# Kernel tuning notes

Measured on AMD Instinct MI355X. Metric: run time of the kernel, lower is better.

## Reference

```python
import jax, jax.numpy as jnp
import numpy as np

LN_EPS = 1e-5

def setup_inputs() -> dict:
    key = jax.random.key(0)
    B, T, D, H, NB = 32, 384, 512, 16, 5  # NB = 5 MHSA blocks actually used
    ks = jax.random.split(key, 10)
    s = 1.0 / np.sqrt(D)
    def w(k, shape):
        return jax.random.normal(k, shape, jnp.float32) * s
    return {
        "x": jax.random.normal(ks[0], (B, T, D), jnp.float32),
        # stacked params for the 5 used MHSA blocks, order:
        # [tmp_attn, layer1_1, layer1_2, layer1_3, layer2_1]
        "qw": w(ks[1], (NB, D, D)), "qb": w(ks[2], (NB, D)),
        "kw": w(ks[3], (NB, D, D)), "kb": w(ks[4], (NB, D)),
        "vw": w(ks[5], (NB, D, D)), "vb": w(ks[6], (NB, D)),
        "temp": jnp.ones((NB, H, 1, 1), jnp.float32),
        "ln_g": jnp.ones((D,), jnp.float32),
        "ln_b": jnp.zeros((D,), jnp.float32),
        "fus_w": w(ks[7], (D, D)), "fus_b": w(ks[8], (D,)),
        "num_heads": H,
    }


def _mhsa(x, wq, bq, wk, bk, wv, bv, temp, H):
    # Faithful to torch: .view(B, H, D//H, T) is a flat reshape of (B,T,D).
    B, T, D = x.shape
    d = D // H
    q = (x @ wq.T + bq).reshape(B, H, d, T)
    k = (x @ wk.T + bk).reshape(B, H, d, T)
    v = (x @ wv.T + bv).reshape(B, H, d, T)
    # k^T @ v -> (B,H,T,T), scaled by per-head temperature, softmax over last dim
    attn = jax.nn.softmax(jnp.einsum("bhdt,bhds->bhts", k, v) * temp, axis=-1)
    out = jnp.einsum("bhdt,bhts->bhds", q, attn)  # (B,H,d,T)
    return out.reshape(B, T, D)


def _layernorm(x, g, b):
    mu = jnp.mean(x, axis=-1, keepdims=True)
    var = jnp.mean(jnp.square(x - mu), axis=-1, keepdims=True)
    return (x - mu) * jax.lax.rsqrt(var + LN_EPS) * g + b


def reference(x, qw, qb, kw, kb, vw, vb, temp, ln_g, ln_b, fus_w, fus_b, num_heads):
    H = num_heads
    blk = lambda i, z: _mhsa(z, qw[i], qb[i], kw[i], kb[i], vw[i], vb[i], temp[i], H)
    x_ = blk(0, x)
    c1, c2, c3 = jnp.split(x, 3, axis=1)
    tmp_layer1 = jnp.concatenate([blk(1, c1), blk(2, c2), blk(3, c3)], axis=1) + x_
    tmp_layer2 = blk(4, _layernorm(tmp_layer1, ln_g, ln_b)) + x_
    alpha = jnp.stack([tmp_layer1, tmp_layer2], axis=0)  # (2,B,T,D)
    alpha = alpha @ fus_w.T + fus_b
    alpha = jax.nn.softmax(alpha, axis=0)
    return tmp_layer1 * alpha[0] + tmp_layer2 * alpha[1]
```

## Files before the change

### kernel.cpp

```cpp
#include <hip/hip_runtime.h>

typedef __attribute__((ext_vector_type(8))) _Float16 half8;
typedef __attribute__((ext_vector_type(4))) _Float16 half4v;
typedef __attribute__((ext_vector_type(4))) float float4v;

__device__ __forceinline__ float4v mfma16x16x32_f16(half8 a, half8 b, float4v c) {
#if defined(__HIP_DEVICE_COMPILE__)
#if __has_builtin(__builtin_amdgcn_mfma_f32_16x16x32_f16)
  return __builtin_amdgcn_mfma_f32_16x16x32_f16(a, b, c, 0, 0, 0);
#elif __has_builtin(__builtin_amdgcn_mfma_f32_16x16x32f16)
  return __builtin_amdgcn_mfma_f32_16x16x32f16(a, b, c, 0, 0, 0);
#else
#error "no 16x16x32 f16 mfma"
#endif
#else
  (void)a; (void)b;
  return c;
#endif
}

__device__ __forceinline__ float4v mfma16x16x16_f16(half4v a, half4v b, float4v c) {
#if defined(__HIP_DEVICE_COMPILE__)
#if __has_builtin(__builtin_amdgcn_mfma_f32_16x16x16f16)
  return __builtin_amdgcn_mfma_f32_16x16x16f16(a, b, c, 0, 0, 0);
#elif __has_builtin(__builtin_amdgcn_mfma_f32_16x16x16_f16)
  return __builtin_amdgcn_mfma_f32_16x16x16_f16(a, b, c, 0, 0, 0);
#else
#error "no 16x16x16 f16 mfma"
#endif
#else
  (void)a; (void)b;
  return c;
#endif
}

__device__ __forceinline__ void gl_lds16(const unsigned short* g, unsigned short* l) {
#if defined(__HIP_DEVICE_COMPILE__)
#if __has_builtin(__builtin_amdgcn_global_load_lds)
  __builtin_amdgcn_global_load_lds(
      (const __attribute__((address_space(1))) unsigned int*)g,
      (__attribute__((address_space(3))) unsigned int*)l, 16, 0, 0);
#else
  *(uint4*)l = *(const uint4*)g;
#endif
#else
  (void)g; (void)l;
#endif
}

__device__ __forceinline__ float fexp2(float x) {
#if defined(__HIP_DEVICE_COMPILE__)
#if __has_builtin(__builtin_amdgcn_exp2f)
  return __builtin_amdgcn_exp2f(x);
#else
  return __expf(x * 0.6931471805599453f);
#endif
#else
  return x;
#endif
}

__device__ __forceinline__ unsigned short f2h(float f) {
  union { _Float16 h; unsigned short u; } v;
  v.h = (_Float16)f;
  return v.u;
}

__global__ __launch_bounds__(256) void cvt_f32_f16(const float* __restrict__ in,
                                                   unsigned short* __restrict__ out, int n4) {
  int i = blockIdx.x * 256 + threadIdx.x;
  if (i >= n4) return;
  float4 v = ((const float4*)in)[i];
  uint2 o;
  o.x = (unsigned)f2h(v.x) | ((unsigned)f2h(v.y) << 16);
  o.y = (unsigned)f2h(v.z) | ((unsigned)f2h(v.w) << 16);
  ((uint2*)out)[i] = o;
}

#define GEMM_K_LOOP(XPTR, WPTR)                                                        \
  const int sw = col & 7;                                                              \
  for (int k0 = 0; k0 < 512; k0 += 64) {                                               \
    const unsigned short* Xg = (XPTR) + k0;                                            \
    const unsigned short* Wg = (WPTR) + k0;                                            \
    _Pragma("unroll") for (int rnd = 0; rnd < 4; ++rnd) {                              \
      const int slot = rnd * 256 + tid;                                                \
      const int r = slot >> 3;                                                         \
      const int c = (slot & 7) ^ (r & 7);                                              \
      gl_lds16(Xg + (size_t)r * 512 + c * 8, &Xs[slot * 8]);                           \
      gl_lds16(Wg + (size_t)r * 512 + c * 8, &Wt[slot * 8]);                           \
    }                                                                                  \
    __syncthreads();                                                                   \
    _Pragma("unroll") for (int kk = 0; kk < 2; ++kk) {                                 \
      half8 af[4], bf[4];                                                              \
      _Pragma("unroll") for (int i = 0; i < 4; ++i) {                                  \
        const int r = wm + i * 16 + col;                                               \
        af[i] = *(const half8*)&Xs[r * 64 + ((kk * 4 + grp) ^ sw) * 8];                \
      }                                                                                \
      _Pragma("unroll") for (int j = 0; j < 4; ++j) {                                  \
        const int r = wn + j * 16 + col;                                               \
        bf[j] = *(const half8*)&Wt[r * 64 + ((kk * 4 + grp) ^ sw) * 8];                \
      }                                                                                \
      _Pragma("unroll") for (int i = 0; i < 4; ++i)                                    \
          _Pragma("unroll") for (int j = 0; j < 4; ++j)                                \
              acc[i][j] = mfma16x16x32_f16(af[i], bf[j], acc[i][j]);                   \
    }                                                                                  \
    __syncthreads();                                                                   \
  }

__global__ __launch_bounds__(256) void gemm_qkv(
    const unsigned short* __restrict__ X,
    const unsigned short* __restrict__ Wq, const unsigned short* __restrict__ Wk,
    const unsigned short* __restrict__ Wv,
    const float* __restrict__ bq, const float* __restrict__ bk, const float* __restrict__ bv,
    unsigned short* __restrict__ Cq, unsigned short* __restrict__ Ck, unsigned short* __restrict__ Cv,
    int wsel_mode, int widx_fixed) {
  const int nt = blockIdx.x, mt = blockIdx.y, z = blockIdx.z;
  const unsigned short* W = (z == 0) ? Wq : ((z == 1) ? Wk : Wv);
  const float* bias = (z == 0) ? bq : ((z == 1) ? bk : bv);
  unsigned short* C = (z == 0) ? Cq : ((z == 1) ? Ck : Cv);
  const int widx = wsel_mode ? (1 + (mt % 3)) : widx_fixed;
  W += (size_t)widx * 512 * 512;
  bias += widx * 512;

  __shared__ __align__(16) unsigned short Xs[128 * 64];
  __shared__ __align__(16) unsigned short Wt[128 * 64];
  const int tid = threadIdx.x, lane = tid & 63, w = tid >> 6;
  const int col = lane & 15, grp = lane >> 4;
  const int wm = (w >> 1) * 64, wn = (w & 1) * 64;

  const float4v zero4 = {0.f, 0.f, 0.f, 0.f};
  float4v acc[4][4];
#pragma unroll
  for (int i = 0; i < 4; ++i)
#pragma unroll
    for (int j = 0; j < 4; ++j) acc[i][j] = zero4;

  GEMM_K_LOOP(X + (size_t)mt * 128 * 512, W + (size_t)nt * 128 * 512)

#pragma unroll
  for (int j = 0; j < 4; ++j) {
    const int n = nt * 128 + wn + j * 16 + col;
    const float bj = bias[n];
#pragma unroll
    for (int i = 0; i < 4; ++i)
#pragma unroll
      for (int r = 0; r < 4; ++r) {
        const int m = mt * 128 + wm + i * 16 + grp * 4 + r;
        C[(size_t)m * 512 + n] = f2h(acc[i][j][r] + bj);
      }
  }
}

__global__ __launch_bounds__(256) void gemm_fusion(
    const unsigned short* __restrict__ X, const unsigned short* __restrict__ Wf,
    const float* __restrict__ tl1, const float* __restrict__ tl2, float* __restrict__ outp) {
  const int nt = blockIdx.x, mt = blockIdx.y;
  __shared__ __align__(16) unsigned short Xs[128 * 64];
  __shared__ __align__(16) unsigned short Wt[128 * 64];
  const int tid = threadIdx.x, lane = tid & 63, w = tid >> 6;
  const int col = lane & 15, grp = lane >> 4;
  const int wm = (w >> 1) * 64, wn = (w & 1) * 64;

  const float4v zero4 = {0.f, 0.f, 0.f, 0.f};
  float4v acc[4][4];
#pragma unroll
  for (int i = 0; i < 4; ++i)
#pragma unroll
    for (int j = 0; j < 4; ++j) acc[i][j] = zero4;

  GEMM_K_LOOP(X + (size_t)mt * 128 * 512, Wf + (size_t)nt * 128 * 512)

#pragma unroll
  for (int j = 0; j < 4; ++j) {
    const int n = nt * 128 + wn + j * 16 + col;
#pragma unroll
    for (int i = 0; i < 4; ++i)
#pragma unroll
      for (int r = 0; r < 4; ++r) {
        const int m = mt * 128 + wm + i * 16 + grp * 4 + r;
        const size_t off = (size_t)m * 512 + n;
        const float t1 = tl1[off], t2 = tl2[off];
        const float sg = 1.0f / (1.0f + __expf(-acc[i][j][r]));
        outp[off] = t2 + (t1 - t2) * sg;
      }
  }
}

template <int T>
__global__ __launch_bounds__(512) void attn_kernel(
    const unsigned short* __restrict__ Qb, const unsigned short* __restrict__ Kb,
    const unsigned short* __restrict__ Vb, const float* __restrict__ temp_base,
    const float* add_src,
    float* outp, int chunk_elems,
    const float* __restrict__ tl1_src, unsigned short* __restrict__ diff_out) {
  constexpr int NT = T / 16;
  constexpr int NSW = (T / 16) / 8;
  constexpr int SLAB = T * 32;
  const int h = blockIdx.x, b = blockIdx.y, cb = blockIdx.z;
  const int base = b * (384 * 512) + cb * chunk_elems + h * SLAB;
  const float tl2e = temp_base[cb * 16 + h] * 1.4426950408889634f;

  __shared__ __align__(16) unsigned short KVt[T][40];
  __shared__ __align__(16) float Zp[2][2][8][16];

  const int tid = threadIdx.x, lane = tid & 63, w = tid >> 6;
  const int col = lane & 15, grp = lane >> 4;

  auto stage = [&](const unsigned short* src) {
    constexpr int ITER = (T * 4) / 512;
#pragma unroll
    for (int p = 0; p < ITER; ++p) {
      const int f = p * 512 + tid;
      const int t = f >> 2, blk = (f & 3) * 8;
      unsigned short tmp[8];
#pragma unroll
      for (int i = 0; i < 8; ++i) tmp[i] = src[(size_t)(blk + i) * T + t];
      *(uint4*)&KVt[t][blk] = *(const uint4*)tmp;
    }
  };

  stage(Vb + base);
  __syncthreads();
  half8 vfr[NSW];
#pragma unroll
  for (int si = 0; si < NSW; ++si)
    vfr[si] = *(const half8*)&KVt[(w + si * 8) * 16 + col][grp * 8];
  __syncthreads();
  stage(Kb + base);
  __syncthreads();

  const float4v zero4 = {0.f, 0.f, 0.f, 0.f};
  const unsigned short* Qsl = Qb + base;
  float4v oacc[NSW][2];
#pragma unroll
  for (int si = 0; si < NSW; ++si) {
    oacc[si][0] = zero4;
    oacc[si][1] = zero4;
  }

  for (int kk = 0; kk < NT / 2; ++kk) {
    const int par = kk & 1;
    float pe[2][NSW][4];
#pragma unroll
    for (int u = 0; u < 2; ++u) {
      const int tt = kk * 2 + u;
      half8 kf = *(const half8*)&KVt[tt * 16 + col][grp * 8];
      float z0 = 0.f, z1 = 0.f, z2 = 0.f, z3 = 0.f;
#pragma unroll
      for (int si = 0; si < NSW; ++si) {
        float4v s = mfma16x16x32_f16(kf, vfr[si], zero4);
        pe[u][si][0] = fexp2(s[0] * tl2e);
        pe[u][si][1] = fexp2(s[1] * tl2e);
        pe[u][si][2] = fexp2(s[2] * tl2e);
        pe[u][si][3] = fexp2(s[3] * tl2e);
        z0 += pe[u][si][0];
        z1 += pe[u][si][1];
        z2 += pe[u][si][2];
        z3 += pe[u][si][3];
      }
#pragma unroll
      for (int m = 1; m < 16; m <<= 1) {
        z0 += __shfl_xor(z0, m);
        z1 += __shfl_xor(z1, m);
        z2 += __shfl_xor(z2, m);
        z3 += __shfl_xor(z3, m);
      }
      if (col == 0) {
        float4v zv = {z0, z1, z2, z3};
        *(float4v*)&Zp[par][u][w][grp * 4] = zv;
      }
    }
    half4v qa[2][2];
#pragma unroll
    for (int u = 0; u < 2; ++u) {
      const int toff = (kk * 2 + u) * 16 + grp * 4;
      qa[u][0] = *(const half4v*)(Qsl + col * T + toff);
      qa[u][1] = *(const half4v*)(Qsl + (16 + col) * T + toff);
    }
    __syncthreads();
#pragma unroll
    for (int u = 0; u < 2; ++u) {
      float4v zs = zero4;
#pragma unroll
      for (int ww = 0; ww < 8; ++ww) zs += *(const float4v*)&Zp[par][u][ww][grp * 4];
      const float zi0 = 1.0f / zs[0], zi1 = 1.0f / zs[1], zi2 = 1.0f / zs[2],
                  zi3 = 1.0f / zs[3];
#pragma unroll
      for (int si = 0; si < NSW; ++si) {
        half4v pb;
        pb[0] = (_Float16)(pe[u][si][0] * zi0);
        pb[1] = (_Float16)(pe[u][si][1] * zi1);
        pb[2] = (_Float16)(pe[u][si][2] * zi2);
        pb[3] = (_Float16)(pe[u][si][3] * zi3);
        oacc[si][0] = mfma16x16x16_f16(qa[u][0], pb, oacc[si][0]);
        oacc[si][1] = mfma16x16x16_f16(qa[u][1], pb, oacc[si][1]);
      }
    }
  }

#pragma unroll
  for (int si = 0; si < NSW; ++si) {
    const int s = (w + si * 8) * 16 + col;
#pragma unroll
    for (int m0 = 0; m0 < 2; ++m0) {
#pragma unroll
      for (int r = 0; r < 4; ++r) {
        const int dd = m0 * 16 + grp * 4 + r;
        const int off = base + dd * T + s;
        float v = oacc[si][m0][r];
        if (add_src) v += add_src[off];
        outp[off] = v;
        if (diff_out) diff_out[off] = f2h(tl1_src[off] - v);
      }
    }
  }
}

__global__ __launch_bounds__(256) void ln_kernel(const float* __restrict__ xin,
                                                 const float* __restrict__ g,
                                                 const float* __restrict__ bb,
                                                 unsigned short* __restrict__ y) {
  const int row = blockIdx.x * 4 + (threadIdx.x >> 6);
  const int lane = threadIdx.x & 63;
  const float* xr = xin + (size_t)row * 512;
  float4 v0 = *(const float4*)&xr[lane * 8];
  float4 v1 = *(const float4*)&xr[lane * 8 + 4];
  float s = v0.x + v0.y + v0.z + v0.w + v1.x + v1.y + v1.z + v1.w;
  float q = v0.x * v0.x + v0.y * v0.y + v0.z * v0.z + v0.w * v0.w +
            v1.x * v1.x + v1.y * v1.y + v1.z * v1.z + v1.w * v1.w;
#pragma unroll
  for (int m = 1; m < 64; m <<= 1) {
    s += __shfl_xor(s, m);
    q += __shfl_xor(q, m);
  }
  const float mean = s * (1.0f / 512.0f);
  const float var = q * (1.0f / 512.0f) - mean * mean;
  const float rs = rsqrtf(var + 1e-5f);
  float4 g0 = *(const float4*)&g[lane * 8];
  float4 g1 = *(const float4*)&g[lane * 8 + 4];
  float4 b0 = *(const float4*)&bb[lane * 8];
  float4 b1 = *(const float4*)&bb[lane * 8 + 4];
  uint4 o;
  o.x = (unsigned)f2h((v0.x - mean) * rs * g0.x + b0.x) |
        ((unsigned)f2h((v0.y - mean) * rs * g0.y + b0.y) << 16);
  o.y = (unsigned)f2h((v0.z - mean) * rs * g0.z + b0.z) |
        ((unsigned)f2h((v0.w - mean) * rs * g0.w + b0.w) << 16);
  o.z = (unsigned)f2h((v1.x - mean) * rs * g1.x + b1.x) |
        ((unsigned)f2h((v1.y - mean) * rs * g1.y + b1.y) << 16);
  o.w = (unsigned)f2h((v1.z - mean) * rs * g1.z + b1.z) |
        ((unsigned)f2h((v1.w - mean) * rs * g1.w + b1.w) << 16);
  *(uint4*)&y[(size_t)row * 512 + lane * 8] = o;
}

extern "C" void kernel_launch(void* const* d_in, const int* in_sizes, int n_in,
                              void* d_out, int out_size, void* d_ws, size_t ws_size,
                              hipStream_t stream) {
  const float* x = (const float*)d_in[0];
  const float* qw = (const float*)d_in[1];
  const float* qb = (const float*)d_in[2];
  const float* kw = (const float*)d_in[3];
  const float* kb = (const float*)d_in[4];
  const float* vw = (const float*)d_in[5];
  const float* vb = (const float*)d_in[6];
  const float* temp = (const float*)d_in[7];
  const float* ln_g = (const float*)d_in[8];
  const float* ln_b = (const float*)d_in[9];
  const float* fus_w = (const float*)d_in[10];
  float* out = (float*)d_out;

  const size_t NE = (size_t)32 * 384 * 512;
  const size_t WE = (size_t)5 * 512 * 512;

  char* p = (char*)d_ws;
  auto alloc = [&](size_t bytes) {
    char* r = p;
    p += (bytes + 255) & ~(size_t)255;
    return r;
  };
  unsigned short* xb = (unsigned short*)alloc(NE * 2);
  unsigned short* wqb = (unsigned short*)alloc(WE * 2);
  unsigned short* wkb = (unsigned short*)alloc(WE * 2);
  unsigned short* wvb = (unsigned short*)alloc(WE * 2);
  unsigned short* fwb = (unsigned short*)alloc((size_t)512 * 512 * 2);
  unsigned short* Qb = (unsigned short*)alloc(NE * 2);
  unsigned short* Kb = (unsigned short*)alloc(NE * 2);
  unsigned short* Vb = (unsigned short*)alloc(NE * 2);
  float* xres = (float*)alloc(NE * 4);
  float* tl1 = (float*)alloc(NE * 4);
  unsigned short* yb = (unsigned short*)alloc(NE * 2);

  cvt_f32_f16<<<(int)((NE / 4 + 255) / 256), 256, 0, stream>>>(x, xb, (int)(NE / 4));
  cvt_f32_f16<<<(int)((WE / 4 + 255) / 256), 256, 0, stream>>>(qw, wqb, (int)(WE / 4));
  cvt_f32_f16<<<(int)((WE / 4 + 255) / 256), 256, 0, stream>>>(kw, wkb, (int)(WE / 4));
  cvt_f32_f16<<<(int)((WE / 4 + 255) / 256), 256, 0, stream>>>(vw, wvb, (int)(WE / 4));
  cvt_f32_f16<<<256, 256, 0, stream>>>(fus_w, fwb, 512 * 512 / 4);

  gemm_qkv<<<dim3(4, 96, 3), 256, 0, stream>>>(xb, wqb, wkb, wvb, qb, kb, vb, Qb, Kb, Vb, 0, 0);
  attn_kernel<384><<<dim3(16, 32, 1), 512, 0, stream>>>(Qb, Kb, Vb, temp, nullptr, xres, 0,
                                                        nullptr, nullptr);
  gemm_qkv<<<dim3(4, 96, 3), 256, 0, stream>>>(xb, wqb, wkb, wvb, qb, kb, vb, Qb, Kb, Vb, 1, 0);
  attn_kernel<128><<<dim3(16, 32, 3), 512, 0, stream>>>(Qb, Kb, Vb, temp + 16, xres, tl1,
                                                        128 * 512, nullptr, nullptr);
  ln_kernel<<<12288 / 4, 256, 0, stream>>>(tl1, ln_g, ln_b, yb);
  gemm_qkv<<<dim3(4, 96, 3), 256, 0, stream>>>(yb, wqb, wkb, wvb, qb, kb, vb, Qb, Kb, Vb, 0, 4);
  attn_kernel<384><<<dim3(16, 32, 1), 512, 0, stream>>>(Qb, Kb, Vb, temp + 64, xres, xres, 0,
                                                        tl1, yb);
  gemm_fusion<<<dim3(4, 96, 1), 256, 0, stream>>>(yb, fwb, tl1, xres, out);

  (void)in_sizes; (void)n_in; (void)out_size; (void)ws_size;
}
```

Before: 413.6 us.

## Enlarge GEMM tiles to 256 rows with 512 threads, batch attention softmax groups

The GEMM kernels now use 512-thread blocks that each compute 256 rows (two 128-row segments that can be non-contiguous, so the per-chunk weight selection is kept) against a 128-column weight tile. This halves the grid and reuses each loaded weight tile across twice as many rows. The attention kernel processes NB t-tiles per barrier group (4 for T=384) instead of 2, cutting syncthreads count, and packs probabilities to f16 with cvt_pkrtz. The larger tiles and groups raise register and LDS pressure and leave fewer blocks to spread across CUs. Round-toward-zero packing slightly changes rounding.

```diff
diff --git a/kernel.cpp b/kernel.cpp
--- a/kernel.cpp
+++ b/kernel.cpp
@@ -2,6 +2,7 @@
 
 typedef __attribute__((ext_vector_type(8))) _Float16 half8;
 typedef __attribute__((ext_vector_type(4))) _Float16 half4v;
+typedef __attribute__((ext_vector_type(2))) _Float16 half2v;
 typedef __attribute__((ext_vector_type(4))) float float4v;
 
 __device__ __forceinline__ float4v mfma16x16x32_f16(half8 a, half8 b, float4v c) {
@@ -57,6 +58,24 @@
 #endif
 #else
   return x;
+#endif
+}
+
+__device__ __forceinline__ half2v pk_f16(float a, float b) {
+#if defined(__HIP_DEVICE_COMPILE__)
+#if __has_builtin(__builtin_amdgcn_cvt_pkrtz)
+  return __builtin_bit_cast(half2v, __builtin_amdgcn_cvt_pkrtz(a, b));
+#else
+  half2v r;
+  r[0] = (_Float16)a;
+  r[1] = (_Float16)b;
+  return r;
+#endif
+#else
+  half2v r;
+  r[0] = (_Float16)a;
+  r[1] = (_Float16)b;
+  return r;
 #endif
 }
 
@@ -77,29 +96,30 @@
   ((uint2*)out)[i] = o;
 }
 
-#define GEMM_K_LOOP(XPTR, WPTR)                                                        \
-  const int sw = col & 7;                                                              \
+#define GEMM_CORE(WGPTR)                                                               \
   for (int k0 = 0; k0 < 512; k0 += 64) {                                               \
-    const unsigned short* Xg = (XPTR) + k0;                                            \
-    const unsigned short* Wg = (WPTR) + k0;                                            \
     _Pragma("unroll") for (int rnd = 0; rnd < 4; ++rnd) {                              \
-      const int slot = rnd * 256 + tid;                                                \
+      const int slot = rnd * 512 + tid;                                                \
       const int r = slot >> 3;                                                         \
       const int c = (slot & 7) ^ (r & 7);                                              \
-      gl_lds16(Xg + (size_t)r * 512 + c * 8, &Xs[slot * 8]);                           \
-      gl_lds16(Wg + (size_t)r * 512 + c * 8, &Wt[slot * 8]);                           \
+      const size_t src = ((r >> 7) ? xrow1 : xrow0) + (size_t)(r & 127) * 512 +        \
+                         (size_t)(k0 + c * 8);                                         \
+      gl_lds16(Xbase + src, &Xs[slot * 8]);                                            \
+    }                                                                                  \
+    _Pragma("unroll") for (int rnd = 0; rnd < 2; ++rnd) {                              \
+      const int s2 = rnd * 512 + tid;                                                  \
+      const int r = s2 >> 3;                                                           \
+      const int c = (s2 & 7) ^ (r & 7);                                                \
+      gl_lds16((WGPTR) + (size_t)r * 512 + k0 + c * 8, &Wt[s2 * 8]);                   \
     }                                                                                  \
     __syncthreads();                                                                   \
     _Pragma("unroll") for (int kk = 0; kk < 2; ++kk) {                                 \
       half8 af[4], bf[4];                                                              \
-      _Pragma("unroll") for (int i = 0; i < 4; ++i) {                                  \
-        const int r = wm + i * 16 + col;                                               \
-        af[i] = *(const half8*)&Xs[r * 64 + ((kk * 4 + grp) ^ sw) * 8];                \
-      }                                                                                \
-      _Pragma("unroll") for (int j = 0; j < 4; ++j) {                                  \
-        const int r = wn + j * 16 + col;                                               \
-        bf[j] = *(const half8*)&Wt[r * 64 + ((kk * 4 + grp) ^ sw) * 8];                \
-      }                                                                                \
+      const int ch = ((kk * 4 + grp) ^ (col & 7)) * 8;                                 \
+      _Pragma("unroll") for (int i = 0; i < 4; ++i)                                    \
+          af[i] = *(const half8*)&Xs[(wm + i * 16 + col) * 64 + ch];                   \
+      _Pragma("unroll") for (int j = 0; j < 4; ++j)                                    \
+          bf[j] = *(const half8*)&Wt[(wn + j * 16 + col) * 64 + ch];                   \
       _Pragma("unroll") for (int i = 0; i < 4; ++i)                                    \
           _Pragma("unroll") for (int j = 0; j < 4; ++j)                                \
               acc[i][j] = mfma16x16x32_f16(af[i], bf[j], acc[i][j]);                   \
@@ -107,7 +127,7 @@
     __syncthreads();                                                                   \
   }
 
-__global__ __launch_bounds__(256) void gemm_qkv(
+__global__ __launch_bounds__(512) void gemm_qkv(
     const unsigned short* __restrict__ X,
     const unsigned short* __restrict__ Wq, const unsigned short* __restrict__ Wk,
     const unsigned short* __restrict__ Wv,
@@ -118,12 +138,18 @@
   const unsigned short* W = (z == 0) ? Wq : ((z == 1) ? Wk : Wv);
   const float* bias = (z == 0) ? bq : ((z == 1) ? bk : bv);
   unsigned short* C = (z == 0) ? Cq : ((z == 1) ? Ck : Cv);
-  const int widx = wsel_mode ? (1 + (mt % 3)) : widx_fixed;
+  const int cpart = mt % 3, bb = (mt / 3) * 2;
+  const int widx = wsel_mode ? (1 + cpart) : widx_fixed;
   W += (size_t)widx * 512 * 512;
   bias += widx * 512;
 
-  __shared__ __align__(16) unsigned short Xs[128 * 64];
-  __shared__ __align__(16) unsigned short Wt[128 * 64];
+  const size_t grow0 = (size_t)bb * 384 + cpart * 128;
+  const size_t grow1 = grow0 + 384;
+  const size_t xrow0 = grow0 * 512, xrow1 = grow1 * 512;
+  const unsigned short* Xbase = X;
+
+  __shared__ __align__(16) unsigned short Xs[2048 * 8];
+  __shared__ __align__(16) unsigned short Wt[1024 * 8];
   const int tid = threadIdx.x, lane = tid & 63, w = tid >> 6;
   const int col = lane & 15, grp = lane >> 4;
   const int wm = (w >> 1) * 64, wn = (w & 1) * 64;
@@ -135,7 +161,7 @@
 #pragma unroll
     for (int j = 0; j < 4; ++j) acc[i][j] = zero4;
 
-  GEMM_K_LOOP(X + (size_t)mt * 128 * 512, W + (size_t)nt * 128 * 512)
+  GEMM_CORE(W + (size_t)nt * 128 * 512)
 
 #pragma unroll
   for (int j = 0; j < 4; ++j) {
@@ -145,18 +171,23 @@
     for (int i = 0; i < 4; ++i)
 #pragma unroll
       for (int r = 0; r < 4; ++r) {
-        const int m = mt * 128 + wm + i * 16 + grp * 4 + r;
-        C[(size_t)m * 512 + n] = f2h(acc[i][j][r] + bj);
-      }
-  }
-}
-
-__global__ __launch_bounds__(256) void gemm_fusion(
+        const int m = wm + i * 16 + grp * 4 + r;
+        const size_t grow = ((m >> 7) ? grow1 : grow0) + (m & 127);
+        C[grow * 512 + n] = f2h(acc[i][j][r] + bj);
+      }
+  }
+}
+
+__global__ __launch_bounds__(512) void gemm_fusion(
     const unsigned short* __restrict__ X, const unsigned short* __restrict__ Wf,
     const float* __restrict__ tl1, const float* __restrict__ tl2, float* __restrict__ outp) {
   const int nt = blockIdx.x, mt = blockIdx.y;
-  __shared__ __align__(16) unsigned short Xs[128 * 64];
-  __shared__ __align__(16) unsigned short Wt[128 * 64];
+  const size_t grow0 = (size_t)mt * 256, grow1 = grow0 + 128;
+  const size_t xrow0 = grow0 * 512, xrow1 = grow1 * 512;
+  const unsigned short* Xbase = X;
+
+  __shared__ __align__(16) unsigned short Xs[2048 * 8];
+  __shared__ __align__(16) unsigned short Wt[1024 * 8];
   const int tid = threadIdx.x, lane = tid & 63, w = tid >> 6;
   const int col = lane & 15, grp = lane >> 4;
   const int wm = (w >> 1) * 64, wn = (w & 1) * 64;
@@ -168,7 +199,7 @@
 #pragma unroll
     for (int j = 0; j < 4; ++j) acc[i][j] = zero4;
 
-  GEMM_K_LOOP(X + (size_t)mt * 128 * 512, Wf + (size_t)nt * 128 * 512)
+  GEMM_CORE(Wf + (size_t)nt * 128 * 512)
 
 #pragma unroll
   for (int j = 0; j < 4; ++j) {
@@ -177,8 +208,8 @@
     for (int i = 0; i < 4; ++i)
 #pragma unroll
       for (int r = 0; r < 4; ++r) {
-        const int m = mt * 128 + wm + i * 16 + grp * 4 + r;
-        const size_t off = (size_t)m * 512 + n;
+        const int m = wm + i * 16 + grp * 4 + r;
+        const size_t off = (((m >> 7) ? grow1 : grow0) + (m & 127)) * 512 + n;
         const float t1 = tl1[off], t2 = tl2[off];
         const float sg = 1.0f / (1.0f + __expf(-acc[i][j][r]));
         outp[off] = t2 + (t1 - t2) * sg;
@@ -186,7 +217,7 @@
   }
 }
 
-template <int T>
+template <int T, int NB>
 __global__ __launch_bounds__(512) void attn_kernel(
     const unsigned short* __restrict__ Qb, const unsigned short* __restrict__ Kb,
     const unsigned short* __restrict__ Vb, const float* __restrict__ temp_base,
@@ -201,7 +232,7 @@
   const float tl2e = temp_base[cb * 16 + h] * 1.4426950408889634f;
 
   __shared__ __align__(16) unsigned short KVt[T][40];
-  __shared__ __align__(16) float Zp[2][2][8][16];
+  __shared__ __align__(16) float Zp[2][NB][8][16];
 
   const int tid = threadIdx.x, lane = tid & 63, w = tid >> 6;
   const int col = lane & 15, grp = lane >> 4;
@@ -238,12 +269,12 @@
     oacc[si][1] = zero4;
   }
 
-  for (int kk = 0; kk < NT / 2; ++kk) {
-    const int par = kk & 1;
-    float pe[2][NSW][4];
-#pragma unroll
-    for (int u = 0; u < 2; ++u) {
-      const int tt = kk * 2 + u;
+  for (int g = 0; g < NT / NB; ++g) {
+    const int par = g & 1;
+    float pe[NB][NSW][4];
+#pragma unroll
+    for (int u = 0; u < NB; ++u) {
+      const int tt = g * NB + u;
       half8 kf = *(const half8*)&KVt[tt * 16 + col][grp * 8];
       float z0 = 0.f, z1 = 0.f, z2 = 0.f, z3 = 0.f;
 #pragma unroll
@@ -270,16 +301,16 @@
         *(float4v*)&Zp[par][u][w][grp * 4] = zv;
       }
     }
-    half4v qa[2][2];
-#pragma unroll
-    for (int u = 0; u < 2; ++u) {
-      const int toff = (kk * 2 + u) * 16 + grp * 4;
+    half4v qa[NB][2];
+#pragma unroll
+    for (int u = 0; u < NB; ++u) {
+      const int toff = (g * NB + u) * 16 + grp * 4;
       qa[u][0] = *(const half4v*)(Qsl + col * T + toff);
       qa[u][1] = *(const half4v*)(Qsl + (16 + col) * T + toff);
     }
     __syncthreads();
 #pragma unroll
-    for (int u = 0; u < 2; ++u) {
+    for (int u = 0; u < NB; ++u) {
       float4v zs = zero4;
 #pragma unroll
       for (int ww = 0; ww < 8; ++ww) zs += *(const float4v*)&Zp[par][u][ww][grp * 4];
@@ -287,11 +318,9 @@
                   zi3 = 1.0f / zs[3];
 #pragma unroll
       for (int si = 0; si < NSW; ++si) {
-        half4v pb;
-        pb[0] = (_Float16)(pe[u][si][0] * zi0);
-        pb[1] = (_Float16)(pe[u][si][1] * zi1);
-        pb[2] = (_Float16)(pe[u][si][2] * zi2);
-        pb[3] = (_Float16)(pe[u][si][3] * zi3);
+        half2v lo = pk_f16(pe[u][si][0] * zi0, pe[u][si][1] * zi1);
+        half2v hi = pk_f16(pe[u][si][2] * zi2, pe[u][si][3] * zi3);
+        half4v pb = __builtin_shufflevector(lo, hi, 0, 1, 2, 3);
         oacc[si][0] = mfma16x16x16_f16(qa[u][0], pb, oacc[si][0]);
         oacc[si][1] = mfma16x16x16_f16(qa[u][1], pb, oacc[si][1]);
       }
@@ -395,17 +424,17 @@
   cvt_f32_f16<<<(int)((WE / 4 + 255) / 256), 256, 0, stream>>>(vw, wvb, (int)(WE / 4));
   cvt_f32_f16<<<256, 256, 0, stream>>>(fus_w, fwb, 512 * 512 / 4);
 
-  gemm_qkv<<<dim3(4, 96, 3), 256, 0, stream>>>(xb, wqb, wkb, wvb, qb, kb, vb, Qb, Kb, Vb, 0, 0);
-  attn_kernel<384><<<dim3(16, 32, 1), 512, 0, stream>>>(Qb, Kb, Vb, temp, nullptr, xres, 0,
-                                                        nullptr, nullptr);
-  gemm_qkv<<<dim3(4, 96, 3), 256, 0, stream>>>(xb, wqb, wkb, wvb, qb, kb, vb, Qb, Kb, Vb, 1, 0);
-  attn_kernel<128><<<dim3(16, 32, 3), 512, 0, stream>>>(Qb, Kb, Vb, temp + 16, xres, tl1,
-                                                        128 * 512, nullptr, nullptr);
+  gemm_qkv<<<dim3(4, 48, 3), 512, 0, stream>>>(xb, wqb, wkb, wvb, qb, kb, vb, Qb, Kb, Vb, 0, 0);
+  attn_kernel<384, 4><<<dim3(16, 32, 1), 512, 0, stream>>>(Qb, Kb, Vb, temp, nullptr, xres, 0,
+                                                           nullptr, nullptr);
+  gemm_qkv<<<dim3(4, 48, 3), 512, 0, stream>>>(xb, wqb, wkb, wvb, qb, kb, vb, Qb, Kb, Vb, 1, 0);
+  attn_kernel<128, 2><<<dim3(16, 32, 3), 512, 0, stream>>>(Qb, Kb, Vb, temp + 16, xres, tl1,
+                                                           128 * 512, nullptr, nullptr);
   ln_kernel<<<12288 / 4, 256, 0, stream>>>(tl1, ln_g, ln_b, yb);
-  gemm_qkv<<<dim3(4, 96, 3), 256, 0, stream>>>(yb, wqb, wkb, wvb, qb, kb, vb, Qb, Kb, Vb, 0, 4);
-  attn_kernel<384><<<dim3(16, 32, 1), 512, 0, stream>>>(Qb, Kb, Vb, temp + 64, xres, xres, 0,
-                                                        tl1, yb);
-  gemm_fusion<<<dim3(4, 96, 1), 256, 0, stream>>>(yb, fwb, tl1, xres, out);
+  gemm_qkv<<<dim3(4, 48, 3), 512, 0, stream>>>(yb, wqb, wkb, wvb, qb, kb, vb, Qb, Kb, Vb, 0, 4);
+  attn_kernel<384, 4><<<dim3(16, 32, 1), 512, 0, stream>>>(Qb, Kb, Vb, temp + 64, xres, xres, 0,
+                                                           tl1, yb);
+  gemm_fusion<<<dim3(4, 48), 512, 0, stream>>>(yb, fwb, tl1, xres, out);
 
   (void)in_sizes; (void)n_in; (void)out_size; (void)ws_size;
 }
```

Result: faster. 404.8 us (-2.1%).
